# Kernel tuning notes

Measured on AMD Instinct MI355X. Metric: run time of the kernel, lower is better.

The kernel has to match this reference:

```python
import jax, jax.numpy as jnp
import numpy as np

N, E, B, P = 50000, 800000, 64, 3
F_E = F_N = F_G = 16
D, H = 64, 128  # embedding/target dim, hidden dim
NEG_SLOPE = 0.01


def _lrelu(z):
    return jax.nn.leaky_relu(z, NEG_SLOPE)


def _mlp3(z, w1, b1, w2, b2, w3, b3):
    z = _lrelu(z @ w1 + b1)
    z = _lrelu(z @ w2 + b2)
    return z @ w3 + b3


def setup_inputs() -> dict:
    key = jax.random.key(0)
    ks = iter(jax.random.split(key, 64))
    s = 0.05

    def lin(i, o, stack=None):
        shp = (i, o) if stack is None else (stack, i, o)
        return jax.random.normal(next(ks), shp, jnp.float32) * s

    def bias(o, stack=None):
        shp = (o,) if stack is None else (stack, o)
        return jax.random.normal(next(ks), shp, jnp.float32) * s

    inp = {}
    inp['x'] = jax.random.normal(next(ks), (N, F_N), jnp.float32)
    inp['edge_attr'] = jax.random.normal(next(ks), (E, F_E), jnp.float32)
    inp['u'] = jax.random.normal(next(ks), (B, F_G), jnp.float32)
    # embeddings
    inp['emb_e_w'], inp['emb_e_b'] = lin(F_E, D), bias(D)
    inp['emb_n_w'], inp['emb_n_b'] = lin(F_N, D), bias(D)
    inp['emb_g_w'], inp['emb_g_b'] = lin(F_G, D), bias(D)
    # message-passing params, stacked over P passes (dims identical since emb==target)
    inp['ew1'], inp['eb1'] = lin(4 * D, H, P), bias(H, P)   # src,dest,edge,global -> 256
    inp['ew2'], inp['eb2'] = lin(H, H, P), bias(H, P)
    inp['ew3'], inp['eb3'] = lin(H, D, P), bias(D, P)
    inp['nw1'], inp['nb1'] = lin(3 * D, H, P), bias(H, P)   # node,edge_agg,global -> 192
    inp['nw2'], inp['nb2'] = lin(H, H, P), bias(H, P)
    inp['nw3'], inp['nb3'] = lin(H, D, P), bias(D, P)
    inp['gw1'], inp['gb1'] = lin(2 * D, H, P), bias(H, P)   # global,node_agg -> 128
    inp['gw2'], inp['gb2'] = lin(H, H, P), bias(H, P)
    inp['gw3'], inp['gb3'] = lin(H, D, P), bias(D, P)
    # decoders
    inp['dec_w'], inp['dec_b'] = lin(D, 1), bias(1)
    inp['vw1'], inp['vb1'] = lin(D, D), bias(D)
    inp['vw2'], inp['vb2'] = lin(D, 1), bias(1)
    # graph structure
    inp['edge_index'] = jax.random.randint(next(ks), (2, E), 0, N, jnp.int32)
    inp['batch'] = jnp.sort(jax.random.randint(next(ks), (N,), 0, B, jnp.int32))
    return inp


def reference(x, edge_attr, u,
              emb_e_w, emb_e_b, emb_n_w, emb_n_b, emb_g_w, emb_g_b,
              ew1, eb1, ew2, eb2, ew3, eb3,
              nw1, nb1, nw2, nb2, nw3, nb3,
              gw1, gb1, gw2, gb2, gw3, gb3,
              dec_w, dec_b, vw1, vb1, vw2, vb2,
              edge_index, batch):
    n_nodes, n_graphs = x.shape[0], u.shape[0]
    row, col = edge_index[0], edge_index[1]

    # embeddings
    e = _lrelu(edge_attr @ emb_e_w + emb_e_b)   # [E, D]
    xh = _lrelu(x @ emb_n_w + emb_n_b)          # [N, D]
    g = _lrelu(u @ emb_g_w + emb_g_b)           # [B, D]

    for p in range(ew1.shape[0]):
        # EdgeModel: gather src/dest/global, MLP
        e_in = jnp.concatenate([xh[row], xh[col], e, g[batch[row]]], axis=1)
        e_new = _mlp3(e_in, ew1[p], eb1[p], ew2[p], eb2[p], ew3[p], eb3[p])
        # NodeModel: scatter_add NEW edge features to dest nodes
        e_agg = jax.ops.segment_sum(e_new, col, num_segments=n_nodes)
        n_in = jnp.concatenate([xh, e_agg, g[batch]], axis=1)
        x_new = _mlp3(n_in, nw1[p], nb1[p], nw2[p], nb2[p], nw3[p], nb3[p])
        # GlobalModel: scatter_add NEW node features per graph
        x_agg = jax.ops.segment_sum(x_new, batch, num_segments=n_graphs)
        g_in = jnp.concatenate([g, x_agg], axis=1)
        g_new = _mlp3(g_in, gw1[p], gb1[p], gw2[p], gb2[p], gw3[p], gb3[p])
        # residual updates
        xh, e, g = xh + x_new, e + e_new, g + g_new

    edge_out = e @ dec_w + dec_b                      # [E, 1]
    value_out = _lrelu(g @ vw1 + vb1) @ vw2 + vb2     # [B, 1]
    return edge_out, value_out
```

## Files before the change

### kernel.cpp

```cpp
#include <hip/hip_runtime.h>
#include <hip/hip_bf16.h>
#include <stdint.h>

typedef unsigned short u16;
typedef unsigned int u32;
typedef short s16x8 __attribute__((ext_vector_type(8)));
typedef float f32x4 __attribute__((ext_vector_type(4)));

#define NN 50000
#define EE 800000
#define BB 64
#define PP 3

__device__ __forceinline__ float b2f(u16 x){ union{u32 u; float f;} c; c.u=((u32)x)<<16; return c.f; }
__device__ __forceinline__ u16 f2b(float v){ union{float f; u32 u;} c; c.f=v; u32 u=c.u; return (u16)((u + 0x7fffu + ((u>>16)&1u))>>16); }
__device__ __forceinline__ float lrelu(float v){ return v>0.f ? v : 0.01f*v; }
__device__ __forceinline__ f32x4 MFMA(s16x8 a, s16x8 b, f32x4 c){
  return __builtin_amdgcn_mfma_f32_16x16x32_bf16(a,b,c,0,0,0);
}

__global__ __launch_bounds__(256) void k_hist(const int* __restrict__ eidx, int* __restrict__ hist){
  int e = blockIdx.x*256 + threadIdx.x;
  if (e < EE) atomicAdd(&hist[eidx[EE+e]], 1);
}

__global__ __launch_bounds__(1024) void k_scan(const int* __restrict__ hist, int* __restrict__ offs){
  __shared__ int lsums[1024];
  const int tid = threadIdx.x;
  const int CH = 49;
  int base = tid*CH;
  int s = 0;
  for (int i=0;i<CH;i++){ int b=base+i; if (b<NN) s += hist[b]; }
  lsums[tid]=s; __syncthreads();
  for (int off=1; off<1024; off<<=1){
    int v = (tid>=off)? lsums[tid-off] : 0;
    __syncthreads();
    lsums[tid] += v;
    __syncthreads();
  }
  int run = (tid>0)? lsums[tid-1] : 0;
  for (int i=0;i<CH;i++){ int b=base+i; if (b<NN){ offs[b]=run; run+=hist[b]; } }
}

__global__ __launch_bounds__(256) void k_scatter(const int* __restrict__ eidx, int* __restrict__ offs,
                                                 int* __restrict__ perm, int* __restrict__ dcols,
                                                 int* __restrict__ inv){
  int e = blockIdx.x*256 + threadIdx.x;
  if (e >= EE) return;
  int col = eidx[EE+e];
  int pos = atomicAdd(&offs[col], 1);
  perm[pos] = e;
  dcols[pos] = col;
  inv[e] = pos;
}

__global__ __launch_bounds__(256) void k_repack(const float* __restrict__ W, u16* __restrict__ out, int K, int Nn){
  int chunks_pp = (K/32)*(Nn/16)*64;
  int t = blockIdx.x*256 + threadIdx.x;
  if (t >= PP*chunks_pp) return;
  int p = t/chunks_pp, rem = t%chunks_pp;
  int NB = Nn/16;
  int kb = rem/(NB*64); int r2 = rem%(NB*64);
  int nb = r2/64; int l = r2&63;
  const float* Wp = W + (size_t)p*K*Nn;
  int k0 = kb*32 + ((l>>4)<<3), n = nb*16 + (l&15);
  u16 tmp[8];
  #pragma unroll
  for (int j=0;j<8;j++) tmp[j] = f2b(Wp[(size_t)(k0+j)*Nn + n]);
  *(uint4*)(out + (size_t)t*8) = *(uint4*)tmp;
}

template<bool SCATTER>
__global__ __launch_bounds__(256) void k_embed(const float* __restrict__ in, const float* __restrict__ W,
                                               const float* __restrict__ b, u16* __restrict__ out, int nrows,
                                               const int* __restrict__ inv){
  __shared__ float wl[1024];
  __shared__ float bl[64];
  int tid = threadIdx.x;
  for (int i=tid;i<1024;i+=256) wl[i]=W[i];
  if (tid<64) bl[tid]=b[tid];
  __syncthreads();
  int row = blockIdx.x*256 + tid;
  if (row >= nrows) return;
  float inb[16];
  const float4* src4=(const float4*)(in + (size_t)row*16);
  #pragma unroll
  for (int q=0;q<4;q++){ float4 v=src4[q]; inb[q*4]=v.x; inb[q*4+1]=v.y; inb[q*4+2]=v.z; inb[q*4+3]=v.w; }
  float acc[64];
  #pragma unroll
  for (int j=0;j<64;j++) acc[j]=bl[j];
  #pragma unroll
  for (int k=0;k<16;k++){
    float a = inb[k];
    const float4* wr4 = (const float4*)(wl + k*64);
    #pragma unroll
    for (int j4=0;j4<16;j4++){
      float4 w4 = wr4[j4];
      acc[j4*4+0] += a*w4.x; acc[j4*4+1] += a*w4.y;
      acc[j4*4+2] += a*w4.z; acc[j4*4+3] += a*w4.w;
    }
  }
  u16 ob[64];
  #pragma unroll
  for (int j=0;j<64;j++) ob[j]=f2b(lrelu(acc[j]));
  int drow = SCATTER ? inv[row] : row;
  uint4* dst=(uint4*)(out + (size_t)drow*64);
  #pragma unroll
  for (int j=0;j<8;j++) dst[j]=((uint4*)ob)[j];
}

__global__ void k_embed_g(const float* __restrict__ in, const float* __restrict__ W, const float* __restrict__ b,
                          u16* __restrict__ g_b, float* __restrict__ g_f){
  __shared__ float wl[1024];
  __shared__ float bl[64];
  int tid = threadIdx.x;
  for (int i=tid;i<1024;i+=64) wl[i]=W[i];
  if (tid<64) bl[tid]=b[tid];
  __syncthreads();
  int row = tid;
  float inb[16];
  const float4* src4=(const float4*)(in + (size_t)row*16);
  #pragma unroll
  for (int q=0;q<4;q++){ float4 v=src4[q]; inb[q*4]=v.x; inb[q*4+1]=v.y; inb[q*4+2]=v.z; inb[q*4+3]=v.w; }
  float acc[64];
  #pragma unroll
  for (int j=0;j<64;j++) acc[j]=bl[j];
  #pragma unroll
  for (int k=0;k<16;k++){
    float a = inb[k];
    const float* wr = wl + k*64;
    #pragma unroll
    for (int j=0;j<64;j++) acc[j] += a*wr[j];
  }
  #pragma unroll
  for (int j=0;j<64;j++){
    float v = lrelu(acc[j]);
    g_f[row*64+j] = v;
    g_b[row*64+j] = f2b(v);
  }
}

__device__ __forceinline__ void rmw16(u16* p, const float* vals){
  uint4 q0=((uint4*)p)[0], q1=((uint4*)p)[1];
  const u16* h0=(const u16*)&q0; const u16* hq=(const u16*)&q1;
  u16 o[16];
  #pragma unroll
  for (int c=0;c<8;c++) o[c]=f2b(b2f(h0[c])+vals[c]);
  #pragma unroll
  for (int c=0;c<8;c++) o[8+c]=f2b(b2f(hq[c])+vals[8+c]);
  ((uint4*)p)[0]=*(uint4*)o; ((uint4*)p)[1]=*(uint4*)(o+8);
}

template<int K0, int MODE, bool LAST>
__global__ __launch_bounds__(256,3) void k_mlp(
    u16* __restrict__ xh_b, u16* __restrict__ e_b,
    float* __restrict__ eagg, float* __restrict__ xagg,
    u16* __restrict__ g_b, float* __restrict__ g_f,
    const int* __restrict__ eidx, const int* __restrict__ batch,
    const int* __restrict__ perm, const int* __restrict__ dcols,
    const uint4* __restrict__ w1f, const uint4* __restrict__ w2f, const uint4* __restrict__ w3f,
    const float* __restrict__ b1, const float* __restrict__ b2, const float* __restrict__ b3,
    const float* __restrict__ dw, const float* __restrict__ db, float* __restrict__ outp)
{
  constexpr int KB  = K0/32;
  constexpr int RS  = K0*2;
  __shared__ __align__(16) char a0[64*RS];
  __shared__ __align__(16) char hbuf[16384];
  __shared__ int s_edge[64];
  __shared__ int s_dcol[64];

  const int tid  = threadIdx.x;
  const int wave = tid>>6, lane = tid&63;
  const int rowbase = blockIdx.x*64;
  const int lrow = lane&15;
  const int lsw  = (lane&7)<<4;
  const int aoff = (lane>>4)*16;
  const int qc   = (lane>>4)*4;

  s16x8 wA[KB][2];
  #pragma unroll
  for (int kb=0;kb<KB;kb++){
    #pragma unroll
    for (int j=0;j<2;j++)
      wA[kb][j] = *(const s16x8*)(w1f + (size_t)(kb*8 + wave*2 + j)*64 + lane);
  }

  {
    const int r = tid>>2, s = tid&3;
    char* drow = a0 + r*RS;
    const int sw = (r&7)<<4;
    if (MODE==0){
      const int slot = rowbase + r;
      const int edge = perm[slot];
      if (s==0){ s_edge[r]=edge; s_dcol[r]=dcols[slot]; }
      const int er = eidx[edge], ec = eidx[EE+edge];
      const u16* src = (s==0)? xh_b + (size_t)er*64
                     : (s==1)? xh_b + (size_t)ec*64
                     : (s==2)? e_b  + (size_t)slot*64
                     :         g_b  + (size_t)batch[er]*64;
      const uint4* s4=(const uint4*)src;
      #pragma unroll
      for (int j=0;j<8;j++)
        *(uint4*)(drow + ((s*128 + j*16) ^ sw)) = s4[j];
    } else if (MODE==1){
      const int node = rowbase + r;
      const bool ok = node < NN;
      if (s==0){
        const uint4* s4=(const uint4*)(xh_b + (size_t)node*64);
        #pragma unroll
        for (int j=0;j<8;j++){ uint4 v={0,0,0,0}; if (ok) v=s4[j];
          *(uint4*)(drow + ((j*16) ^ sw)) = v; }
      } else if (s==1){
        const float4* s4=(const float4*)(eagg + (size_t)node*64);
        #pragma unroll
        for (int j=0;j<8;j++){
          u16 tmp[8]={0,0,0,0,0,0,0,0};
          if (ok){ float4 lo=s4[2*j], hi=s4[2*j+1];
            tmp[0]=f2b(lo.x);tmp[1]=f2b(lo.y);tmp[2]=f2b(lo.z);tmp[3]=f2b(lo.w);
            tmp[4]=f2b(hi.x);tmp[5]=f2b(hi.y);tmp[6]=f2b(hi.z);tmp[7]=f2b(hi.w); }
          *(uint4*)(drow + ((128 + j*16) ^ sw)) = *(uint4*)tmp;
        }
      } else if (s==2){
        int bidx = ok ? batch[node] : 0;
        const uint4* s4=(const uint4*)(g_b + (size_t)bidx*64);
        #pragma unroll
        for (int j=0;j<8;j++){ uint4 v={0,0,0,0}; if (ok) v=s4[j];
          *(uint4*)(drow + ((256 + j*16) ^ sw)) = v; }
      }
    } else {
      if (s==0){
        const uint4* s4=(const uint4*)(g_b + (size_t)r*64);
        #pragma unroll
        for (int j=0;j<8;j++) *(uint4*)(drow + ((j*16) ^ sw)) = s4[j];
      } else if (s==1){
        const float4* s4=(const float4*)(xagg + (size_t)r*64);
        #pragma unroll
        for (int j=0;j<8;j++){
          u16 tmp[8];
          float4 lo=s4[2*j], hi=s4[2*j+1];
          tmp[0]=f2b(lo.x);tmp[1]=f2b(lo.y);tmp[2]=f2b(lo.z);tmp[3]=f2b(lo.w);
          tmp[4]=f2b(hi.x);tmp[5]=f2b(hi.y);tmp[6]=f2b(hi.z);tmp[7]=f2b(hi.w);
          *(uint4*)(drow + ((128 + j*16) ^ sw)) = *(uint4*)tmp;
        }
      }
    }
  }
  __syncthreads();

  f32x4 acc[4][2];
  #pragma unroll
  for (int rb=0;rb<4;rb++){ acc[rb][0]=f32x4{0,0,0,0}; acc[rb][1]=f32x4{0,0,0,0}; }
  #pragma unroll
  for (int kb=0;kb<KB;kb++){
    #pragma unroll
    for (int rb=0;rb<4;rb++){
      s16x8 af = *(const s16x8*)(a0 + (rb*16+lrow)*RS + ((kb*64 + aoff) ^ lsw));
      acc[rb][0] = MFMA(wA[kb][0], af, acc[rb][0]);
      acc[rb][1] = MFMA(wA[kb][1], af, acc[rb][1]);
    }
  }

  s16x8 wB[4][2];
  #pragma unroll
  for (int kb=0;kb<4;kb++){
    #pragma unroll
    for (int j=0;j<2;j++)
      wB[kb][j] = *(const s16x8*)(w2f + (size_t)(kb*8 + wave*2 + j)*64 + lane);
  }

  #pragma unroll
  for (int j=0;j<2;j++){
    const float4 bs = *(const float4*)(b1 + wave*32 + j*16 + qc);
    #pragma unroll
    for (int rb=0;rb<4;rb++){
      int row = rb*16 + lrow;
      int c2 = (wave*32 + j*16 + qc)*2;
      u16 t0=f2b(lrelu(acc[rb][j][0]+bs.x)), t1=f2b(lrelu(acc[rb][j][1]+bs.y));
      u16 t2=f2b(lrelu(acc[rb][j][2]+bs.z)), t3=f2b(lrelu(acc[rb][j][3]+bs.w));
      uint2 pk = make_uint2((u32)t0 | ((u32)t1<<16), (u32)t2 | ((u32)t3<<16));
      *(uint2*)(hbuf + row*256 + (c2 ^ ((row&7)<<4))) = pk;
    }
  }
  __syncthreads();

  f32x4 acc2[4][2];
  #pragma unroll
  for (int rb=0;rb<4;rb++){ acc2[rb][0]=f32x4{0,0,0,0}; acc2[rb][1]=f32x4{0,0,0,0}; }
  #pragma unroll
  for (int kb=0;kb<4;kb++){
    #pragma unroll
    for (int rb=0;rb<4;rb++){
      s16x8 af = *(const s16x8*)(hbuf + (rb*16+lrow)*256 + ((kb*64 + aoff) ^ lsw));
      acc2[rb][0] = MFMA(wB[kb][0], af, acc2[rb][0]);
      acc2[rb][1] = MFMA(wB[kb][1], af, acc2[rb][1]);
    }
  }

  s16x8 wC[4];
  #pragma unroll
  for (int kb=0;kb<4;kb++)
    wC[kb] = *(const s16x8*)(w3f + (size_t)(kb*4 + wave)*64 + lane);

  #pragma unroll
  for (int j=0;j<2;j++){
    const float4 bs = *(const float4*)(b2 + wave*32 + j*16 + qc);
    #pragma unroll
    for (int rb=0;rb<4;rb++){
      int row = rb*16 + lrow;
      int c2 = (wave*32 + j*16 + qc)*2;
      u16 t0=f2b(lrelu(acc2[rb][j][0]+bs.x)), t1=f2b(lrelu(acc2[rb][j][1]+bs.y));
      u16 t2=f2b(lrelu(acc2[rb][j][2]+bs.z)), t3=f2b(lrelu(acc2[rb][j][3]+bs.w));
      uint2 pk = make_uint2((u32)t0 | ((u32)t1<<16), (u32)t2 | ((u32)t3<<16));
      *(uint2*)(a0 + row*256 + (c2 ^ ((row&7)<<4))) = pk;
    }
  }
  __syncthreads();

  f32x4 acc3[4];
  #pragma unroll
  for (int rb=0;rb<4;rb++) acc3[rb]=f32x4{0,0,0,0};
  #pragma unroll
  for (int kb=0;kb<4;kb++){
    #pragma unroll
    for (int rb=0;rb<4;rb++){
      s16x8 af = *(const s16x8*)(a0 + (rb*16+lrow)*256 + ((kb*64 + aoff) ^ lsw));
      acc3[rb] = MFMA(wC[kb], af, acc3[rb]);
    }
  }
  {
    const float4 b3v = *(const float4*)(b3 + wave*16 + qc);
    #pragma unroll
    for (int rb=0;rb<4;rb++){
      int row = rb*16 + lrow;
      int c4 = (wave*16 + qc)*4;
      float4 o = make_float4(acc3[rb][0]+b3v.x, acc3[rb][1]+b3v.y, acc3[rb][2]+b3v.z, acc3[rb][3]+b3v.w);
      *(float4*)(hbuf + row*256 + (c4 ^ ((row&7)<<4))) = o;
    }
  }
  __syncthreads();

  const int r2 = tid>>2, cs = (tid&3)*16;
  const int rsw2 = (r2&7)<<4;
  if (MODE==0){
    const int slot = rowbase + r2;
    float vals[16];
    #pragma unroll
    for (int c=0;c<16;c++) vals[c]=*(const float*)(hbuf + r2*256 + (((cs+c)*4)^rsw2));
    if (LAST){
      const int edge = s_edge[r2];
      u16* p = e_b + (size_t)slot*64 + cs;
      uint4 q0=((uint4*)p)[0], q1=((uint4*)p)[1];
      const u16* h0=(const u16*)&q0; const u16* hq=(const u16*)&q1;
      float dwl[16];
      const float4* dw4 = (const float4*)(dw + cs);
      #pragma unroll
      for (int q=0;q<4;q++){ float4 v=dw4[q]; dwl[q*4]=v.x; dwl[q*4+1]=v.y; dwl[q*4+2]=v.z; dwl[q*4+3]=v.w; }
      u16 o[16]; float part=0.f;
      #pragma unroll
      for (int c=0;c<8;c++){ u16 nb16=f2b(b2f(h0[c])+vals[c]); o[c]=nb16; part += b2f(nb16)*dwl[c]; }
      #pragma unroll
      for (int c=0;c<8;c++){ u16 nb16=f2b(b2f(hq[c])+vals[8+c]); o[8+c]=nb16; part += b2f(nb16)*dwl[8+c]; }
      ((uint4*)p)[0]=*(uint4*)o; ((uint4*)p)[1]=*(uint4*)(o+8);
      part += __shfl_xor(part,1);
      part += __shfl_xor(part,2);
      if ((tid&3)==0) outp[edge] = part + db[0];
    } else {
      rmw16(e_b + (size_t)slot*64 + cs, vals);
    }
    const int col64 = tid&63, rg = tid>>6;
    float ssum = 0.f; int cur = -1;
    #pragma unroll
    for (int rr=0;rr<16;rr++){
      int row = rg*16+rr;
      int gid = s_dcol[row];
      float v = *(const float*)(hbuf + row*256 + ((col64*4) ^ ((row&7)<<4)));
      if (gid != cur){ if (cur>=0) unsafeAtomicAdd(eagg + (size_t)cur*64 + col64, ssum); ssum=0.f; cur=gid; }
      ssum += v;
    }
    if (cur>=0) unsafeAtomicAdd(eagg + (size_t)cur*64 + col64, ssum);
  } else if (MODE==1){
    const int node = rowbase + r2;
    if (node < NN){
      float vals[16];
      #pragma unroll
      for (int c=0;c<16;c++) vals[c]=*(const float*)(hbuf + r2*256 + (((cs+c)*4)^rsw2));
      rmw16(xh_b + (size_t)node*64 + cs, vals);
    }
    const int col = tid&63, rg = tid>>6;
    float s = 0.f; int cur = -1;
    for (int rr=0;rr<16;rr++){
      int row = rg*16+rr; int nd = rowbase+row;
      int gid = (nd<NN) ? batch[nd] : -1;
      float v = *(const float*)(hbuf + row*256 + ((col*4) ^ ((row&7)<<4)));
      if (gid != cur){ if (cur>=0) unsafeAtomicAdd(xagg + cur*64 + col, s); s=0.f; cur=gid; }
      if (gid>=0) s += v;
    }
    if (cur>=0) unsafeAtomicAdd(xagg + cur*64 + col, s);
  } else {
    float vals[16];
    #pragma unroll
    for (int c=0;c<16;c++) vals[c]=*(const float*)(hbuf + r2*256 + (((cs+c)*4)^rsw2));
    #pragma unroll
    for (int c=0;c<16;c++){
      int idx = r2*64 + cs + c;
      float nv = g_f[idx] + vals[c];
      g_f[idx] = nv; g_b[idx] = f2b(nv);
    }
  }
}

__global__ void k_value(const float* __restrict__ g_f, const float* __restrict__ vw1, const float* __restrict__ vb1,
                        const float* __restrict__ vw2, const float* __restrict__ vb2, float* __restrict__ out){
  __shared__ float w1[4096];
  __shared__ float b1s[64];
  __shared__ float w2[64];
  int tid=threadIdx.x;
  for (int i=tid;i<4096;i+=64) w1[i]=vw1[i];
  if (tid<64){ b1s[tid]=vb1[tid]; w2[tid]=vw2[tid]; }
  __syncthreads();
  float gi[64];
  #pragma unroll
  for (int k=0;k<64;k++) gi[k]=g_f[tid*64+k];
  float val=vb2[0];
  for (int j=0;j<64;j++){
    float s=b1s[j];
    #pragma unroll
    for (int k=0;k<64;k++) s+=gi[k]*w1[k*64+j];
    val += lrelu(s)*w2[j];
  }
  out[tid]=val;
}

extern "C" void kernel_launch(void* const* d_in, const int* in_sizes, int n_in,
                              void* d_out, int out_size, void* d_ws, size_t ws_size,
                              hipStream_t stream){
  const float* x    =(const float*)d_in[0];
  const float* ea   =(const float*)d_in[1];
  const float* uu   =(const float*)d_in[2];
  const float* eew  =(const float*)d_in[3];
  const float* eeb  =(const float*)d_in[4];
  const float* enw  =(const float*)d_in[5];
  const float* enb  =(const float*)d_in[6];
  const float* egw  =(const float*)d_in[7];
  const float* egb  =(const float*)d_in[8];
  const float* ew1  =(const float*)d_in[9];
  const float* eb1  =(const float*)d_in[10];
  const float* ew2  =(const float*)d_in[11];
  const float* eb2  =(const float*)d_in[12];
  const float* ew3  =(const float*)d_in[13];
  const float* eb3  =(const float*)d_in[14];
  const float* nw1  =(const float*)d_in[15];
  const float* nb1  =(const float*)d_in[16];
  const float* nw2  =(const float*)d_in[17];
  const float* nb2  =(const float*)d_in[18];
  const float* nw3  =(const float*)d_in[19];
  const float* nb3  =(const float*)d_in[20];
  const float* gw1  =(const float*)d_in[21];
  const float* gb1  =(const float*)d_in[22];
  const float* gw2  =(const float*)d_in[23];
  const float* gb2  =(const float*)d_in[24];
  const float* gw3  =(const float*)d_in[25];
  const float* gb3  =(const float*)d_in[26];
  const float* dw   =(const float*)d_in[27];
  const float* db   =(const float*)d_in[28];
  const float* vw1  =(const float*)d_in[29];
  const float* vb1  =(const float*)d_in[30];
  const float* vw2  =(const float*)d_in[31];
  const float* vb2  =(const float*)d_in[32];
  const int* eidx =(const int*)d_in[33];
  const int* batch=(const int*)d_in[34];

  char* ws=(char*)d_ws; size_t off=0;
  auto alloc=[&](size_t b)->char*{ char* p=ws+off; off=(off+b+255)&~(size_t)255; return p; };
  u16*   xh_b =(u16*)  alloc((size_t)NN*64*2);
  u16*   e_s  =(u16*)  alloc((size_t)EE*64*2);
  float* eagg =(float*)alloc((size_t)NN*64*4);
  float* xagg =(float*)alloc((size_t)BB*64*4);
  u16*   g_bb =(u16*)  alloc((size_t)BB*64*2);
  float* g_f  =(float*)alloc((size_t)BB*64*4);
  u16* ew1f=(u16*)alloc((size_t)PP*4096*16);
  u16* ew2f=(u16*)alloc((size_t)PP*2048*16);
  u16* ew3f=(u16*)alloc((size_t)PP*1024*16);
  u16* nw1f=(u16*)alloc((size_t)PP*3072*16);
  u16* nw2f=(u16*)alloc((size_t)PP*2048*16);
  u16* nw3f=(u16*)alloc((size_t)PP*1024*16);
  u16* gw1f=(u16*)alloc((size_t)PP*2048*16);
  u16* gw2f=(u16*)alloc((size_t)PP*2048*16);
  u16* gw3f=(u16*)alloc((size_t)PP*1024*16);
  int* hist =(int*)alloc((size_t)NN*4);
  int* offs =(int*)alloc((size_t)NN*4);
  int* perm =(int*)alloc((size_t)EE*4);
  int* dcols=(int*)alloc((size_t)EE*4);
  int* inv  =(int*)alloc((size_t)EE*4);
  float* out=(float*)d_out;

  hipMemsetAsync(hist, 0, (size_t)NN*4, stream);
  k_hist<<<(EE+255)/256,256,0,stream>>>(eidx, hist);
  k_scan<<<1,1024,0,stream>>>(hist, offs);
  k_scatter<<<(EE+255)/256,256,0,stream>>>(eidx, offs, perm, dcols, inv);

  auto rp=[&](const float* W, u16* dst, int K, int Nn){
    int total = PP*(K/32)*(Nn/16)*64;
    k_repack<<<(total+255)/256,256,0,stream>>>(W,dst,K,Nn);
  };
  rp(ew1,ew1f,256,128); rp(ew2,ew2f,128,128); rp(ew3,ew3f,128,64);
  rp(nw1,nw1f,192,128); rp(nw2,nw2f,128,128); rp(nw3,nw3f,128,64);
  rp(gw1,gw1f,128,128); rp(gw2,gw2f,128,128); rp(gw3,gw3f,128,64);

  k_embed<true ><<<(EE+255)/256,256,0,stream>>>(ea, eew, eeb, e_s, EE, inv);
  k_embed<false><<<(NN+255)/256,256,0,stream>>>(x,  enw, enb, xh_b, NN, nullptr);
  k_embed_g<<<1,64,0,stream>>>(uu, egw, egb, g_bb, g_f);

  for (int p=0;p<PP;p++){
    hipMemsetAsync(eagg, 0, (size_t)NN*64*4, stream);
    hipMemsetAsync(xagg, 0, (size_t)BB*64*4, stream);
    if (p<PP-1)
      k_mlp<256,0,false><<<EE/64,256,0,stream>>>(xh_b,e_s,eagg,xagg,g_bb,g_f,eidx,batch,perm,dcols,
          (const uint4*)ew1f + (size_t)p*4096, (const uint4*)ew2f + (size_t)p*2048, (const uint4*)ew3f + (size_t)p*1024,
          eb1+p*128, eb2+p*128, eb3+p*64, dw, db, out);
    else
      k_mlp<256,0,true><<<EE/64,256,0,stream>>>(xh_b,e_s,eagg,xagg,g_bb,g_f,eidx,batch,perm,dcols,
          (const uint4*)ew1f + (size_t)p*4096, (const uint4*)ew2f + (size_t)p*2048, (const uint4*)ew3f + (size_t)p*1024,
          eb1+p*128, eb2+p*128, eb3+p*64, dw, db, out);
    k_mlp<192,1,false><<<(NN+63)/64,256,0,stream>>>(xh_b,e_s,eagg,xagg,g_bb,g_f,eidx,batch,perm,dcols,
        (const uint4*)nw1f + (size_t)p*3072, (const uint4*)nw2f + (size_t)p*2048, (const uint4*)nw3f + (size_t)p*1024,
        nb1+p*128, nb2+p*128, nb3+p*64, dw, db, out);
    k_mlp<128,2,false><<<1,256,0,stream>>>(xh_b,e_s,eagg,xagg,g_bb,g_f,eidx,batch,perm,dcols,
        (const uint4*)gw1f + (size_t)p*2048, (const uint4*)gw2f + (size_t)p*2048, (const uint4*)gw3f + (size_t)p*1024,
        gb1+p*128, gb2+p*128, gb3+p*64, dw, db, out);
  }
  k_value<<<1,64,0,stream>>>(g_f, vw1, vb1, vw2, vb2, out+EE);
}
```

Measured before the change: 1.204 ms.

## Alias MLP LDS buffers, raise occupancy to 4, and XCD-swizzle block order

The k_mlp kernel's separate hbuf scratch is merged into the a0 input buffer, with an extra barrier so the hidden activations can overwrite the already-consumed input. This cuts shared memory per block, and launch bounds are raised to 4 blocks per CU to use that headroom for occupancy. Edge and node blocks are also remapped so consecutive row tiles land on the same XCD, which may improve L2 locality for the CSR-sorted scatter-adds. The risks are register spilling under the tighter occupancy bound, plus one more barrier per block.

New measurement: 1.160 ms. -3.6%, faster.

```diff
diff --git a/kernel.cpp b/kernel.cpp
--- a/kernel.cpp
+++ b/kernel.cpp
@@ -17,6 +17,12 @@
 __device__ __forceinline__ float lrelu(float v){ return v>0.f ? v : 0.01f*v; }
 __device__ __forceinline__ f32x4 MFMA(s16x8 a, s16x8 b, f32x4 c){
   return __builtin_amdgcn_mfma_f32_16x16x32_bf16(a,b,c,0,0,0);
+}
+
+__device__ __forceinline__ int xcd_swz(int bid, int nwg){
+  int q = nwg>>3, r = nwg&7;
+  int x = bid&7, i = bid>>3;
+  return (x<r ? x*(q+1) : r*(q+1)+(x-r)*q) + i;
 }
 
 __global__ __launch_bounds__(256) void k_hist(const int* __restrict__ eidx, int* __restrict__ hist){
@@ -152,7 +158,7 @@
 }
 
 template<int K0, int MODE, bool LAST>
-__global__ __launch_bounds__(256,3) void k_mlp(
+__global__ __launch_bounds__(256,4) void k_mlp(
     u16* __restrict__ xh_b, u16* __restrict__ e_b,
     float* __restrict__ eagg, float* __restrict__ xagg,
     u16* __restrict__ g_b, float* __restrict__ g_f,
@@ -164,14 +170,17 @@
 {
   constexpr int KB  = K0/32;
   constexpr int RS  = K0*2;
-  __shared__ __align__(16) char a0[64*RS];
-  __shared__ __align__(16) char hbuf[16384];
+  constexpr int A0SZ = (64*RS > 32768) ? 64*RS : 32768;
+  __shared__ __align__(16) char a0[A0SZ];
   __shared__ int s_edge[64];
   __shared__ int s_dcol[64];
+  char* h1 = a0;
+  char* h2 = a0 + 16384;
+  char* h3 = a0;
 
   const int tid  = threadIdx.x;
   const int wave = tid>>6, lane = tid&63;
-  const int rowbase = blockIdx.x*64;
+  const int rowbase = (MODE==2 ? blockIdx.x : xcd_swz(blockIdx.x, gridDim.x))*64;
   const int lrow = lane&15;
   const int lsw  = (lane&7)<<4;
   const int aoff = (lane>>4)*16;
@@ -267,6 +276,7 @@
     for (int j=0;j<2;j++)
       wB[kb][j] = *(const s16x8*)(w2f + (size_t)(kb*8 + wave*2 + j)*64 + lane);
   }
+  __syncthreads();
 
   #pragma unroll
   for (int j=0;j<2;j++){
@@ -278,7 +288,7 @@
       u16 t0=f2b(lrelu(acc[rb][j][0]+bs.x)), t1=f2b(lrelu(acc[rb][j][1]+bs.y));
       u16 t2=f2b(lrelu(acc[rb][j][2]+bs.z)), t3=f2b(lrelu(acc[rb][j][3]+bs.w));
       uint2 pk = make_uint2((u32)t0 | ((u32)t1<<16), (u32)t2 | ((u32)t3<<16));
-      *(uint2*)(hbuf + row*256 + (c2 ^ ((row&7)<<4))) = pk;
+      *(uint2*)(h1 + row*256 + (c2 ^ ((row&7)<<4))) = pk;
     }
   }
   __syncthreads();
@@ -290,7 +300,7 @@
   for (int kb=0;kb<4;kb++){
     #pragma unroll
     for (int rb=0;rb<4;rb++){
-      s16x8 af = *(const s16x8*)(hbuf + (rb*16+lrow)*256 + ((kb*64 + aoff) ^ lsw));
+      s16x8 af = *(const s16x8*)(h1 + (rb*16+lrow)*256 + ((kb*64 + aoff) ^ lsw));
       acc2[rb][0] = MFMA(wB[kb][0], af, acc2[rb][0]);
       acc2[rb][1] = MFMA(wB[kb][1], af, acc2[rb][1]);
     }
@@ -311,7 +321,7 @@
       u16 t0=f2b(lrelu(acc2[rb][j][0]+bs.x)), t1=f2b(lrelu(acc2[rb][j][1]+bs.y));
       u16 t2=f2b(lrelu(acc2[rb][j][2]+bs.z)), t3=f2b(lrelu(acc2[rb][j][3]+bs.w));
       uint2 pk = make_uint2((u32)t0 | ((u32)t1<<16), (u32)t2 | ((u32)t3<<16));
-      *(uint2*)(a0 + row*256 + (c2 ^ ((row&7)<<4))) = pk;
+      *(uint2*)(h2 + row*256 + (c2 ^ ((row&7)<<4))) = pk;
     }
   }
   __syncthreads();
@@ -323,7 +333,7 @@
   for (int kb=0;kb<4;kb++){
     #pragma unroll
     for (int rb=0;rb<4;rb++){
-      s16x8 af = *(const s16x8*)(a0 + (rb*16+lrow)*256 + ((kb*64 + aoff) ^ lsw));
+      s16x8 af = *(const s16x8*)(h2 + (rb*16+lrow)*256 + ((kb*64 + aoff) ^ lsw));
       acc3[rb] = MFMA(wC[kb], af, acc3[rb]);
     }
   }
@@ -334,7 +344,7 @@
       int row = rb*16 + lrow;
       int c4 = (wave*16 + qc)*4;
       float4 o = make_float4(acc3[rb][0]+b3v.x, acc3[rb][1]+b3v.y, acc3[rb][2]+b3v.z, acc3[rb][3]+b3v.w);
-      *(float4*)(hbuf + row*256 + (c4 ^ ((row&7)<<4))) = o;
+      *(float4*)(h3 + row*256 + (c4 ^ ((row&7)<<4))) = o;
     }
   }
   __syncthreads();
@@ -345,7 +355,7 @@
     const int slot = rowbase + r2;
     float vals[16];
     #pragma unroll
-    for (int c=0;c<16;c++) vals[c]=*(const float*)(hbuf + r2*256 + (((cs+c)*4)^rsw2));
+    for (int c=0;c<16;c++) vals[c]=*(const float*)(h3 + r2*256 + (((cs+c)*4)^rsw2));
     if (LAST){
       const int edge = s_edge[r2];
       u16* p = e_b + (size_t)slot*64 + cs;
@@ -373,7 +383,7 @@
     for (int rr=0;rr<16;rr++){
       int row = rg*16+rr;
       int gid = s_dcol[row];
-      float v = *(const float*)(hbuf + row*256 + ((col64*4) ^ ((row&7)<<4)));
+      float v = *(const float*)(h3 + row*256 + ((col64*4) ^ ((row&7)<<4)));
       if (gid != cur){ if (cur>=0) unsafeAtomicAdd(eagg + (size_t)cur*64 + col64, ssum); ssum=0.f; cur=gid; }
       ssum += v;
     }
@@ -383,7 +393,7 @@
     if (node < NN){
       float vals[16];
       #pragma unroll
-      for (int c=0;c<16;c++) vals[c]=*(const float*)(hbuf + r2*256 + (((cs+c)*4)^rsw2));
+      for (int c=0;c<16;c++) vals[c]=*(const float*)(h3 + r2*256 + (((cs+c)*4)^rsw2));
       rmw16(xh_b + (size_t)node*64 + cs, vals);
     }
     const int col = tid&63, rg = tid>>6;
@@ -391,7 +401,7 @@
     for (int rr=0;rr<16;rr++){
       int row = rg*16+rr; int nd = rowbase+row;
       int gid = (nd<NN) ? batch[nd] : -1;
-      float v = *(const float*)(hbuf + row*256 + ((col*4) ^ ((row&7)<<4)));
+      float v = *(const float*)(h3 + row*256 + ((col*4) ^ ((row&7)<<4)));
       if (gid != cur){ if (cur>=0) unsafeAtomicAdd(xagg + cur*64 + col, s); s=0.f; cur=gid; }
       if (gid>=0) s += v;
     }
@@ -399,7 +409,7 @@
   } else {
     float vals[16];
     #pragma unroll
-    for (int c=0;c<16;c++) vals[c]=*(const float*)(hbuf + r2*256 + (((cs+c)*4)^rsw2));
+    for (int c=0;c<16;c++) vals[c]=*(const float*)(h3 + r2*256 + (((cs+c)*4)^rsw2));
     #pragma unroll
     for (int c=0;c<16;c++){
       int idx = r2*64 + cs + c;
```
